# Kernel tuning notes

Measured on AMD Instinct MI355X. Metric: run time of the kernel, lower is better.

The kernel has to match this reference:

```python
import jax, jax.numpy as jnp
import numpy as np

B, NUM_OBJ, R, D, C = 1024, 128, 32, 512, 7  # scans, obj slots, rel samples, feat dim, rel classes
N = NUM_OBJ + R  # 160 graph nodes per scan


def setup_inputs() -> dict:
    key = jax.random.key(0)
    ks = jax.random.split(key, 8)
    obj_feats = jax.random.normal(ks[0], (B, NUM_OBJ, D), jnp.float32)
    pairs = jax.random.randint(ks[1], (B, R, 2), 0, NUM_OBJ, dtype=jnp.int32)
    init = lambda k, shape, fan_in: jax.random.normal(k, shape, jnp.float32) / np.float32(np.sqrt(fan_in))
    return {
        "obj_feats": obj_feats,
        "pairs": pairs,
        "fuse_w": init(ks[2], (2 * D, D), 2 * D), "fuse_b": jnp.zeros((D,), jnp.float32),
        "gcn_w": init(ks[3], (D, D), D), "gcn_b": jnp.zeros((D,), jnp.float32),
        "fc1_w": init(ks[4], (D, 256), D), "fc1_b": jnp.zeros((256,), jnp.float32),
        "fc2_w": init(ks[5], (256, 128), 256), "fc2_b": jnp.zeros((128,), jnp.float32),
        "fc3_w": init(ks[6], (128, C), 128), "fc3_b": jnp.zeros((C,), jnp.float32),
    }


def reference(obj_feats, pairs, fuse_w, fuse_b, gcn_w, gcn_b,
              fc1_w, fc1_b, fc2_w, fc2_b, fc3_w, fc3_b):
    # --- init_rel_node (pos_fuse=False): fuse sub/obj features per sampled pair ---
    sub = jnp.take_along_axis(obj_feats, pairs[:, :, 0:1], axis=1)  # [B,R,D]
    obj = jnp.take_along_axis(obj_feats, pairs[:, :, 1:2], axis=1)  # [B,R,D]
    init_rel = jnp.concatenate([sub, obj], axis=-1) @ fuse_w + fuse_b  # [B,R,D]

    # --- X: object node feats in rows [0,NUM_OBJ), rel node feats in rows [NUM_OBJ,N) ---
    X = jnp.concatenate([obj_feats, init_rel], axis=1)  # [B,N,D]

    # --- A: get_graph_gcn_with_rel -- scatter 4 directed edges per pair ---
    b_idx = jnp.arange(B)[:, None]                      # [B,1]
    ridx = NUM_OBJ + jnp.arange(R)[None, :]             # [1,R] rel node index j+num_obj
    p0, p1 = pairs[:, :, 0], pairs[:, :, 1]             # [B,R]
    A = jnp.zeros((B, N, N), jnp.float32)
    A = A.at[b_idx, p0, ridx].set(1.0)
    A = A.at[b_idx, ridx, p1].set(1.0)
    A = A.at[b_idx, p1, ridx].set(1.0)
    A = A.at[b_idx, ridx, p0].set(1.0)

    # --- simpleGCN: relu((A @ X) W + b) ---
    H = jax.nn.relu(jnp.einsum('bnm,bmd->bnd', A, X) @ gcn_w + gcn_b)  # [B,N,D]

    # --- residual: GCN rel-node output + init rel feats ---
    rel_feat = H[:, NUM_OBJ:, :] + init_rel  # [B,R,D]

    # --- proxi_detector (dropout = identity, eval behavior) ---
    h = jax.nn.relu(rel_feat @ fc1_w + fc1_b)
    h = jax.nn.relu(h @ fc2_w + fc2_b)
    logits = h @ fc3_w + fc3_b  # [B,R,C]
    return jax.nn.softmax(logits, axis=-1)
```

## Files before the change

kernel.cpp:

```cpp
#include <hip/hip_runtime.h>
#include <hip/hip_bf16.h>

#define B_    1024
#define NOBJ  128
#define RREL  32
#define DIM   512
#define MTOT  32768

typedef __bf16 bf16x8 __attribute__((ext_vector_type(8)));
typedef float  f32x4  __attribute__((ext_vector_type(4)));
typedef unsigned short us;
typedef unsigned short us8v __attribute__((ext_vector_type(8)));

__device__ __forceinline__ us f2bf(float f) {
    unsigned int u = __float_as_uint(f);
    u += 0x7FFFu + ((u >> 16) & 1u);
    return (us)(u >> 16);
}
__device__ __forceinline__ float bf2f(us h) {
    return __uint_as_float(((unsigned int)h) << 16);
}

__device__ __forceinline__ void load16_to_lds(const us* g, us* l) {
    __builtin_amdgcn_global_load_lds((const __attribute__((address_space(1))) void*)g,
                                     (__attribute__((address_space(3))) void*)l,
                                     16, 0, 0);
}

__global__ __launch_bounds__(256) void prep_weights(
        const float* __restrict__ fw, const float* __restrict__ gw,
        const float* __restrict__ w1, const float* __restrict__ w2,
        us* __restrict__ WfT, us* __restrict__ WgT,
        us* __restrict__ W1T, us* __restrict__ W2T) {
    __shared__ float t32[32][33];
    int id = blockIdx.x;
    const float* in; us* out; int K, N, local;
    if (id < 512)      { in = fw; out = WfT; K = 1024; N = 512; local = id; }
    else if (id < 768) { in = gw; out = WgT; K = 512;  N = 512; local = id - 512; }
    else if (id < 896) { in = w1; out = W1T; K = 512;  N = 256; local = id - 768; }
    else               { in = w2; out = W2T; K = 256;  N = 128; local = id - 896; }
    int tilesN = N >> 5;
    int bk = (local / tilesN) * 32;
    int bn = (local % tilesN) * 32;
    int t  = threadIdx.x;
    int tx = t & 31, ty = t >> 5;
#pragma unroll
    for (int i = 0; i < 4; ++i)
        t32[ty + i * 8][tx] = in[(size_t)(bk + ty + i * 8) * N + bn + tx];
    __syncthreads();
#pragma unroll
    for (int i = 0; i < 4; ++i)
        out[(size_t)(bn + ty + i * 8) * K + bk + tx] = f2bf(t32[tx][ty + i * 8]);
}

__global__ __launch_bounds__(512, 2) void gemm_fused12(
        const float* __restrict__ obj,
        const int*   __restrict__ pairs,
        const us* __restrict__ WfT,
        const us* __restrict__ WgT,
        const float* __restrict__ fuse_b, const float* __restrict__ gcn_b,
        us* __restrict__ rf) {
    __shared__ __align__(16) us ldsA[2][4096];
    __shared__ __align__(16) us ldsB[2][16384];

    int tid  = threadIdx.x;
    int wid  = tid >> 6;
    int lane = tid & 63;
    int wm   = wid >> 2;
    int wn   = wid & 3;
    int m0   = blockIdx.x * 128;

    f32x4 acc[4][8];
#pragma unroll
    for (int i = 0; i < 4; ++i)
#pragma unroll
        for (int j = 0; j < 8; ++j)
#pragma unroll
            for (int k = 0; k < 4; ++k) acc[i][j][k] = 0.0f;

    int r = tid >> 2, c = tid & 3;
    int m  = m0 + r;
    int p0 = pairs[2 * m + 0];
    int p1 = pairs[2 * m + 1];
    int bi = m >> 5;
    const float* sP = obj + (size_t)(bi * NOBJ + p0) * DIM + c * 8;
    const float* oP = obj + (size_t)(bi * NOBJ + p1) * DIM + c * 8;
    float osc = (p0 != p1) ? 1.0f : 0.0f;

    int l15  = lane & 15;
    int koff = (lane >> 4) * 8;
    int aoff = (wm * 64  + l15) * 32 + koff;
    int boff = (wn * 128 + l15) * 32 + koff;

    float bg_[8], bf_[8];
#pragma unroll
    for (int j = 0; j < 8; ++j) {
        int col = wn * 128 + j * 16 + l15;
        bg_[j] = gcn_b[col];
        bf_[j] = fuse_b[col];
    }

    us* aDst0 = &ldsA[0][r * 32 + c * 8];
    us* aDst1 = &ldsA[1][r * 32 + c * 8];

    auto compute = [&](int buf) {
        bf16x8 a[4], b[8];
#pragma unroll
        for (int i = 0; i < 4; ++i)
            a[i] = *(const bf16x8*)(&ldsA[buf][aoff + i * 512]);
#pragma unroll
        for (int j = 0; j < 8; ++j)
            b[j] = *(const bf16x8*)(&ldsB[buf][boff + j * 512]);
#pragma unroll
        for (int i = 0; i < 4; ++i)
#pragma unroll
            for (int j = 0; j < 8; ++j)
                acc[i][j] = __builtin_amdgcn_mfma_f32_16x16x32_bf16(a[i], b[j], acc[i][j], 0, 0, 0);
    };

    {
        float4 sa = *(const float4*)(sP);
        float4 sb = *(const float4*)(sP + 4);
        float4 oa = *(const float4*)(oP);
        float4 ob = *(const float4*)(oP + 4);
        us8v u;
        u[0] = f2bf(fmaf(osc, oa.x, sa.x)); u[1] = f2bf(fmaf(osc, oa.y, sa.y));
        u[2] = f2bf(fmaf(osc, oa.z, sa.z)); u[3] = f2bf(fmaf(osc, oa.w, sa.w));
        u[4] = f2bf(fmaf(osc, ob.x, sb.x)); u[5] = f2bf(fmaf(osc, ob.y, sb.y));
        u[6] = f2bf(fmaf(osc, ob.z, sb.z)); u[7] = f2bf(fmaf(osc, ob.w, sb.w));
        *(us8v*)aDst0 = u;
#pragma unroll
        for (int q = 0; q < 4; ++q)
            load16_to_lds(WgT + (size_t)(q * 128 + r) * 512 + c * 8,
                          &ldsB[0][q * 4096 + tid * 8]);
    }
    __syncthreads();

    int cur = 0;
    for (int t = 0; t < 48; ++t) {
        float4 ra, rb, rc, rd;
        int  nt = t + 1;
        bool hv = nt < 48;
        bool gm = nt < 16;
        if (hv) {
            if (gm) {
                int k0 = nt * 32;
                ra = *(const float4*)(sP + k0);
                rb = *(const float4*)(sP + k0 + 4);
                rc = *(const float4*)(oP + k0);
                rd = *(const float4*)(oP + k0 + 4);
#pragma unroll
                for (int q = 0; q < 4; ++q)
                    load16_to_lds(WgT + (size_t)(q * 128 + r) * 512 + k0 + c * 8,
                                  &ldsB[cur ^ 1][q * 4096 + tid * 8]);
            } else {
                int kf = (nt - 16) * 32;
                const float* p = (kf < 512) ? (sP + kf) : (oP + (kf - 512));
                ra = *(const float4*)(p);
                rb = *(const float4*)(p + 4);
#pragma unroll
                for (int q = 0; q < 4; ++q)
                    load16_to_lds(WfT + (size_t)(q * 128 + r) * 1024 + kf + c * 8,
                                  &ldsB[cur ^ 1][q * 4096 + tid * 8]);
            }
        }

        compute(cur);

        if (t == 15) {
#pragma unroll
            for (int i = 0; i < 4; ++i)
#pragma unroll
                for (int j = 0; j < 8; ++j)
#pragma unroll
                    for (int k = 0; k < 4; ++k)
                        acc[i][j][k] = fmaxf(acc[i][j][k] + bg_[j], 0.0f);
        }

        if (hv) {
            us8v u;
            if (gm) {
                u[0] = f2bf(fmaf(osc, rc.x, ra.x)); u[1] = f2bf(fmaf(osc, rc.y, ra.y));
                u[2] = f2bf(fmaf(osc, rc.z, ra.z)); u[3] = f2bf(fmaf(osc, rc.w, ra.w));
                u[4] = f2bf(fmaf(osc, rd.x, rb.x)); u[5] = f2bf(fmaf(osc, rd.y, rb.y));
                u[6] = f2bf(fmaf(osc, rd.z, rb.z)); u[7] = f2bf(fmaf(osc, rd.w, rb.w));
            } else {
                u[0] = f2bf(ra.x); u[1] = f2bf(ra.y); u[2] = f2bf(ra.z); u[3] = f2bf(ra.w);
                u[4] = f2bf(rb.x); u[5] = f2bf(rb.y); u[6] = f2bf(rb.z); u[7] = f2bf(rb.w);
            }
            *(us8v*)((cur == 0) ? aDst1 : aDst0) = u;
        }
        __syncthreads();
        cur ^= 1;
    }

    int crow = wm * 64 + (lane >> 4) * 4;
#pragma unroll
    for (int i = 0; i < 4; ++i)
#pragma unroll
        for (int j = 0; j < 8; ++j) {
            int col = wn * 128 + j * 16 + l15;
#pragma unroll
            for (int jj = 0; jj < 4; ++jj) {
                int row = m0 + crow + i * 16 + jj;
                rf[(size_t)row * 512 + col] = f2bf(acc[i][j][jj] + bf_[j]);
            }
        }
}

#define H1S 264
#define H2S 136
__global__ __launch_bounds__(256, 2) void tail_kernel(
        const us* __restrict__ rf,
        const us* __restrict__ W1T,
        const us* __restrict__ W2T,
        const float* __restrict__ b1, const float* __restrict__ b2,
        const float* __restrict__ w3, const float* __restrict__ b3,
        float* __restrict__ out) {
    __shared__ __align__(16) unsigned char pool[57888];
    us*    sA   = (us*)(pool);
    us*    sB   = (us*)(pool + 4096);
    us*    sH2  = (us*)(pool);
    us*    sH1  = (us*)(pool + 20480);
    float* sRed = (float*)(pool + 20480);
    float* sW3  = (float*)(pool + 54272);
    float* sB3  = (float*)(pool + 57856);

    int tid  = threadIdx.x;
    int wid  = tid >> 6;
    int lane = tid & 63;
    int m0   = blockIdx.x * 64;

    for (int i = tid; i < 128 * 7; i += 256) sW3[i] = w3[i];
    if (tid < 7) sB3[tid] = b3[tid];

    int r = tid >> 2, c = tid & 3;
    int koff = (lane >> 4) * 8;
    int l15  = lane & 15;

    f32x4 acc1[4][4];
#pragma unroll
    for (int i = 0; i < 4; ++i)
#pragma unroll
        for (int j = 0; j < 4; ++j)
#pragma unroll
            for (int k = 0; k < 4; ++k) acc1[i][j][k] = 0.0f;

    {
        const us* ag = rf + (size_t)(m0 + r) * 512 + c * 8;
        us* la = sA + wid * 512;
        for (int k0 = 0; k0 < 512; k0 += 32) {
            __syncthreads();
            load16_to_lds(ag + k0, la);
#pragma unroll
            for (int q = 0; q < 4; ++q)
                load16_to_lds(W1T + (size_t)(q * 64 + r) * 512 + k0 + c * 8,
                              sB + q * 2048 + wid * 512);
            __syncthreads();
            bf16x8 a[4], b[4];
#pragma unroll
            for (int i = 0; i < 4; ++i)
                a[i] = *(const bf16x8*)(sA + (l15 + i * 16) * 32 + koff);
#pragma unroll
            for (int j = 0; j < 4; ++j)
                b[j] = *(const bf16x8*)(sB + (wid * 64 + j * 16 + l15) * 32 + koff);
#pragma unroll
            for (int i = 0; i < 4; ++i)
#pragma unroll
                for (int j = 0; j < 4; ++j)
                    acc1[i][j] = __builtin_amdgcn_mfma_f32_16x16x32_bf16(a[i], b[j], acc1[i][j], 0, 0, 0);
        }
    }
#pragma unroll
    for (int i = 0; i < 4; ++i)
#pragma unroll
        for (int j = 0; j < 4; ++j) {
            int col = wid * 64 + j * 16 + l15;
            float bb = b1[col];
#pragma unroll
            for (int jj = 0; jj < 4; ++jj) {
                int row = i * 16 + (lane >> 4) * 4 + jj;
                sH1[row * H1S + col] = f2bf(fmaxf(acc1[i][j][jj] + bb, 0.0f));
            }
        }

    int nw = wid & 1, kw = wid >> 1;
    f32x4 acc2[4][4];
#pragma unroll
    for (int i = 0; i < 4; ++i)
#pragma unroll
        for (int j = 0; j < 4; ++j)
#pragma unroll
            for (int k = 0; k < 4; ++k) acc2[i][j][k] = 0.0f;

    for (int t = 0; t < 4; ++t) {
        __syncthreads();
#pragma unroll
        for (int s = 0; s < 2; ++s)
#pragma unroll
            for (int q = 0; q < 2; ++q)
                load16_to_lds(W2T + (size_t)(q * 64 + r) * 256 + s * 128 + t * 32 + c * 8,
                              sB + s * 4096 + q * 2048 + wid * 512);
        __syncthreads();
        bf16x8 a[4], b[4];
#pragma unroll
        for (int i = 0; i < 4; ++i)
            a[i] = *(const bf16x8*)(sH1 + (l15 + i * 16) * H1S + kw * 128 + t * 32 + koff);
#pragma unroll
        for (int j = 0; j < 4; ++j)
            b[j] = *(const bf16x8*)(sB + kw * 4096 + (nw * 64 + j * 16 + l15) * 32 + koff);
#pragma unroll
        for (int i = 0; i < 4; ++i)
#pragma unroll
            for (int j = 0; j < 4; ++j)
                acc2[i][j] = __builtin_amdgcn_mfma_f32_16x16x32_bf16(a[i], b[j], acc2[i][j], 0, 0, 0);
    }
    __syncthreads();
    if (kw == 1) {
#pragma unroll
        for (int i = 0; i < 4; ++i)
#pragma unroll
            for (int j = 0; j < 4; ++j) {
                int col = nw * 64 + j * 16 + l15;
#pragma unroll
                for (int jj = 0; jj < 4; ++jj) {
                    int row = i * 16 + (lane >> 4) * 4 + jj;
                    sRed[row * 132 + col] = acc2[i][j][jj];
                }
            }
    }
    __syncthreads();
    if (kw == 0) {
#pragma unroll
        for (int i = 0; i < 4; ++i)
#pragma unroll
            for (int j = 0; j < 4; ++j) {
                int col = nw * 64 + j * 16 + l15;
                float bb = b2[col];
#pragma unroll
                for (int jj = 0; jj < 4; ++jj) {
                    int row = i * 16 + (lane >> 4) * 4 + jj;
                    float v = acc2[i][j][jj] + sRed[row * 132 + col] + bb;
                    sH2[row * H2S + col] = f2bf(fmaxf(v, 0.0f));
                }
            }
    }
    __syncthreads();

    int row = tid >> 2;
    int p   = tid & 3;
    float accv[7];
#pragma unroll
    for (int cc = 0; cc < 7; ++cc) accv[cc] = 0.0f;
    const us* hrow = sH2 + row * H2S + p * 32;
    for (int kk = 0; kk < 8; ++kk) {
        ushort4 u = *(const ushort4*)(hrow + kk * 4);
        float f0 = bf2f(u.x), f1 = bf2f(u.y), f2 = bf2f(u.z), f3 = bf2f(u.w);
        int k = p * 32 + kk * 4;
#pragma unroll
        for (int cc = 0; cc < 7; ++cc) {
            accv[cc] = fmaf(f0, sW3[(k + 0) * 7 + cc], accv[cc]);
            accv[cc] = fmaf(f1, sW3[(k + 1) * 7 + cc], accv[cc]);
            accv[cc] = fmaf(f2, sW3[(k + 2) * 7 + cc], accv[cc]);
            accv[cc] = fmaf(f3, sW3[(k + 3) * 7 + cc], accv[cc]);
        }
    }
#pragma unroll
    for (int cc = 0; cc < 7; ++cc) {
        accv[cc] += __shfl_xor(accv[cc], 1);
        accv[cc] += __shfl_xor(accv[cc], 2);
    }
    if (p == 0) {
        float mx = accv[0] + sB3[0];
        float lg[7];
#pragma unroll
        for (int cc = 0; cc < 7; ++cc) { lg[cc] = accv[cc] + sB3[cc]; mx = fmaxf(mx, lg[cc]); }
        float sum = 0.f;
#pragma unroll
        for (int cc = 0; cc < 7; ++cc) { lg[cc] = __expf(lg[cc] - mx); sum += lg[cc]; }
        float inv = 1.0f / sum;
#pragma unroll
        for (int cc = 0; cc < 7; ++cc) out[(size_t)(m0 + row) * 7 + cc] = lg[cc] * inv;
    }
}

extern "C" void kernel_launch(void* const* d_in, const int* in_sizes, int n_in,
                              void* d_out, int out_size, void* d_ws, size_t ws_size,
                              hipStream_t stream) {
    (void)in_sizes; (void)n_in; (void)out_size; (void)ws_size;
    const float* obj    = (const float*)d_in[0];
    const int*   pairs  = (const int*)  d_in[1];
    const float* fuse_w = (const float*)d_in[2];
    const float* fuse_b = (const float*)d_in[3];
    const float* gcn_w  = (const float*)d_in[4];
    const float* gcn_b  = (const float*)d_in[5];
    const float* fc1_w  = (const float*)d_in[6];
    const float* fc1_b  = (const float*)d_in[7];
    const float* fc2_w  = (const float*)d_in[8];
    const float* fc2_b  = (const float*)d_in[9];
    const float* fc3_w  = (const float*)d_in[10];
    const float* fc3_b  = (const float*)d_in[11];
    float* out = (float*)d_out;

    char* ws = (char*)d_ws;
    us* rf   = (us*)(ws);
    us* WfT  = (us*)(ws + (32u << 20));
    us* WgT  = (us*)(ws + (33u << 20));
    us* W1T  = (us*)(ws + (34u << 20));
    us* W2T  = (us*)(ws + (35u << 20));

    prep_weights<<<928, 256, 0, stream>>>(fuse_w, gcn_w, fc1_w, fc2_w,
                                          WfT, WgT, W1T, W2T);

    gemm_fused12<<<MTOT / 128, 512, 0, stream>>>(
        obj, pairs, WfT, WgT, fuse_b, gcn_b, rf);

    tail_kernel<<<MTOT / 64, 256, 0, stream>>>(
        rf, W1T, W2T, fc1_b, fc2_b, fc3_w, fc3_b, out);
}
```

Baseline: 425.8 us.

## Shrink fused GEMM to 64-row blocks and double-buffer tail fc1 loads

The fused gemm kernel moves from 128-row tiles with 8 waves to 64-row tiles with 4 waves, each wave owning a 128-column slice. This doubles the grid to 512 blocks, which spreads better across CUs, but each block now streams the full weight tile for half as many rows. The tail kernel's fc1 loop gains double-buffered LDS staging so the next K-slice's async loads overlap the MFMAs, with one barrier per step instead of two. The larger LDS pool in the tail kernel may reduce occupancy.

```diff
diff --git a/kernel.cpp b/kernel.cpp
--- a/kernel.cpp
+++ b/kernel.cpp
@@ -53,22 +53,20 @@
         out[(size_t)(bn + ty + i * 8) * K + bk + tx] = f2bf(t32[tx][ty + i * 8]);
 }
 
-__global__ __launch_bounds__(512, 2) void gemm_fused12(
+__global__ __launch_bounds__(256, 2) void gemm_fused12(
         const float* __restrict__ obj,
         const int*   __restrict__ pairs,
         const us* __restrict__ WfT,
         const us* __restrict__ WgT,
         const float* __restrict__ fuse_b, const float* __restrict__ gcn_b,
         us* __restrict__ rf) {
-    __shared__ __align__(16) us ldsA[2][4096];
+    __shared__ __align__(16) us ldsA[2][2048];
     __shared__ __align__(16) us ldsB[2][16384];
 
     int tid  = threadIdx.x;
     int wid  = tid >> 6;
     int lane = tid & 63;
-    int wm   = wid >> 2;
-    int wn   = wid & 3;
-    int m0   = blockIdx.x * 128;
+    int m0   = blockIdx.x * 64;
 
     f32x4 acc[4][8];
 #pragma unroll
@@ -89,19 +87,19 @@
 
     int l15  = lane & 15;
     int koff = (lane >> 4) * 8;
-    int aoff = (wm * 64  + l15) * 32 + koff;
-    int boff = (wn * 128 + l15) * 32 + koff;
+    int aoff = l15 * 32 + koff;
+    int boff = (wid * 128 + l15) * 32 + koff;
 
     float bg_[8], bf_[8];
 #pragma unroll
     for (int j = 0; j < 8; ++j) {
-        int col = wn * 128 + j * 16 + l15;
+        int col = wid * 128 + j * 16 + l15;
         bg_[j] = gcn_b[col];
         bf_[j] = fuse_b[col];
     }
 
-    us* aDst0 = &ldsA[0][r * 32 + c * 8];
-    us* aDst1 = &ldsA[1][r * 32 + c * 8];
+    us* aDst0 = &ldsA[0][tid * 8];
+    us* aDst1 = &ldsA[1][tid * 8];
 
     auto compute = [&](int buf) {
         bf16x8 a[4], b[8];
@@ -130,9 +128,9 @@
         u[6] = f2bf(fmaf(osc, ob.z, sb.z)); u[7] = f2bf(fmaf(osc, ob.w, sb.w));
         *(us8v*)aDst0 = u;
 #pragma unroll
-        for (int q = 0; q < 4; ++q)
-            load16_to_lds(WgT + (size_t)(q * 128 + r) * 512 + c * 8,
-                          &ldsB[0][q * 4096 + tid * 8]);
+        for (int q = 0; q < 8; ++q)
+            load16_to_lds(WgT + (size_t)(q * 64 + r) * 512 + c * 8,
+                          &ldsB[0][q * 2048 + tid * 8]);
     }
     __syncthreads();
 
@@ -150,18 +148,18 @@
                 rc = *(const float4*)(oP + k0);
                 rd = *(const float4*)(oP + k0 + 4);
 #pragma unroll
-                for (int q = 0; q < 4; ++q)
-                    load16_to_lds(WgT + (size_t)(q * 128 + r) * 512 + k0 + c * 8,
-                                  &ldsB[cur ^ 1][q * 4096 + tid * 8]);
+                for (int q = 0; q < 8; ++q)
+                    load16_to_lds(WgT + (size_t)(q * 64 + r) * 512 + k0 + c * 8,
+                                  &ldsB[cur ^ 1][q * 2048 + tid * 8]);
             } else {
                 int kf = (nt - 16) * 32;
                 const float* p = (kf < 512) ? (sP + kf) : (oP + (kf - 512));
                 ra = *(const float4*)(p);
                 rb = *(const float4*)(p + 4);
 #pragma unroll
-                for (int q = 0; q < 4; ++q)
-                    load16_to_lds(WfT + (size_t)(q * 128 + r) * 1024 + kf + c * 8,
-                                  &ldsB[cur ^ 1][q * 4096 + tid * 8]);
+                for (int q = 0; q < 8; ++q)
+                    load16_to_lds(WfT + (size_t)(q * 64 + r) * 1024 + kf + c * 8,
+                                  &ldsB[cur ^ 1][q * 2048 + tid * 8]);
             }
         }
 
@@ -194,12 +192,12 @@
         cur ^= 1;
     }
 
-    int crow = wm * 64 + (lane >> 4) * 4;
+    int crow = (lane >> 4) * 4;
 #pragma unroll
     for (int i = 0; i < 4; ++i)
 #pragma unroll
         for (int j = 0; j < 8; ++j) {
-            int col = wn * 128 + j * 16 + l15;
+            int col = wid * 128 + j * 16 + l15;
 #pragma unroll
             for (int jj = 0; jj < 4; ++jj) {
                 int row = m0 + crow + i * 16 + jj;
@@ -217,14 +215,14 @@
         const float* __restrict__ b1, const float* __restrict__ b2,
         const float* __restrict__ w3, const float* __restrict__ b3,
         float* __restrict__ out) {
-    __shared__ __align__(16) unsigned char pool[57888];
+    __shared__ __align__(16) unsigned char pool[78368];
     us*    sA   = (us*)(pool);
-    us*    sB   = (us*)(pool + 4096);
+    us*    sB   = (us*)(pool + 8192);
     us*    sH2  = (us*)(pool);
-    us*    sH1  = (us*)(pool + 20480);
-    float* sRed = (float*)(pool + 20480);
-    float* sW3  = (float*)(pool + 54272);
-    float* sB3  = (float*)(pool + 57856);
+    us*    sH1  = (us*)(pool + 40960);
+    float* sRed = (float*)(pool + 40960);
+    float* sW3  = (float*)(pool + 74752);
+    float* sB3  = (float*)(pool + 78336);
 
     int tid  = threadIdx.x;
     int wid  = tid >> 6;
@@ -248,27 +246,32 @@
 
     {
         const us* ag = rf + (size_t)(m0 + r) * 512 + c * 8;
-        us* la = sA + wid * 512;
-        for (int k0 = 0; k0 < 512; k0 += 32) {
-            __syncthreads();
-            load16_to_lds(ag + k0, la);
+        auto stage1 = [&](int k0, int b) {
+            load16_to_lds(ag + k0, sA + b * 2048 + wid * 512);
 #pragma unroll
             for (int q = 0; q < 4; ++q)
                 load16_to_lds(W1T + (size_t)(q * 64 + r) * 512 + k0 + c * 8,
-                              sB + q * 2048 + wid * 512);
-            __syncthreads();
+                              sB + b * 8192 + q * 2048 + wid * 512);
+        };
+        stage1(0, 0);
+        __syncthreads();
+        int cur = 0;
+        for (int s = 0; s < 16; ++s) {
+            if (s < 15) stage1((s + 1) * 32, cur ^ 1);
             bf16x8 a[4], b[4];
 #pragma unroll
             for (int i = 0; i < 4; ++i)
-                a[i] = *(const bf16x8*)(sA + (l15 + i * 16) * 32 + koff);
+                a[i] = *(const bf16x8*)(sA + cur * 2048 + (l15 + i * 16) * 32 + koff);
 #pragma unroll
             for (int j = 0; j < 4; ++j)
-                b[j] = *(const bf16x8*)(sB + (wid * 64 + j * 16 + l15) * 32 + koff);
+                b[j] = *(const bf16x8*)(sB + cur * 8192 + (wid * 64 + j * 16 + l15) * 32 + koff);
 #pragma unroll
             for (int i = 0; i < 4; ++i)
 #pragma unroll
                 for (int j = 0; j < 4; ++j)
                     acc1[i][j] = __builtin_amdgcn_mfma_f32_16x16x32_bf16(a[i], b[j], acc1[i][j], 0, 0, 0);
+            __syncthreads();
+            cur ^= 1;
         }
     }
 #pragma unroll
@@ -412,7 +415,7 @@
     prep_weights<<<928, 256, 0, stream>>>(fuse_w, gcn_w, fc1_w, fc2_w,
                                           WfT, WgT, W1T, W2T);
 
-    gemm_fused12<<<MTOT / 128, 512, 0, stream>>>(
+    gemm_fused12<<<MTOT / 64, 256, 0, stream>>>(
         obj, pairs, WfT, WgT, fuse_b, gcn_b, rf);
 
     tail_kernel<<<MTOT / 64, 256, 0, stream>>>(
```

New measurement: 427.5 us. No clear change (+0.4%).
